# Performance work log

Hardware: AMD Instinct MI355X
Metric: run time of the kernel (lower is better)

The kernel has to match this reference:

```python
import jax, jax.numpy as jnp
import numpy as np

T, B, D_IN, H = 512, 128, 1024, 2048

def _lstm_cell(x, h, c, W_ih, W_hh, b):
    # PyTorch LSTMCell gate order: i, f, g, o
    gates = x @ W_ih.T + h @ W_hh.T + b  # [B, 4H]
    i, f, g, o = jnp.split(gates, 4, axis=-1)
    c_new = jax.nn.sigmoid(f) * c + jax.nn.sigmoid(i) * jnp.tanh(g)
    h_new = jax.nn.sigmoid(o) * jnp.tanh(c_new)
    return h_new, c_new

def setup_inputs() -> dict:
    key = jax.random.key(0)
    ks = jax.random.split(key, 12)
    k = 1.0 / np.sqrt(H)  # torch LSTMCell init range
    u = lambda kk, shape: jax.random.uniform(kk, shape, jnp.float32, -k, k)
    return {
        "input_seq": jax.random.normal(ks[0], (T, B, D_IN), jnp.float32),
        "h0": jax.random.normal(ks[1], (2, B, H), jnp.float32),
        "c0": jax.random.normal(ks[2], (2, B, H), jnp.float32),
        "W_ih0": u(ks[3], (4 * H, D_IN)),
        "W_hh0": u(ks[4], (4 * H, H)),
        "b0": u(ks[5], (4 * H,)),
        "W_ih1": u(ks[6], (4 * H, H)),
        "W_hh1": u(ks[7], (4 * H, H)),
        "b1": u(ks[8], (4 * H,)),
    }

def reference(input_seq, h0, c0, W_ih0, W_hh0, b0, W_ih1, W_hh1, b1):
    def step(carry, x_t):
        h0_, c0_, h1_, c1_ = carry
        h0n, c0n = _lstm_cell(x_t, h0_, c0_, W_ih0, W_hh0, b0)
        h1n, c1n = _lstm_cell(h0n, h1_, c1_, W_ih1, W_hh1, b1)
        return (h0n, c0n, h1n, c1n), None

    init = (h0[0], c0[0], h0[1], c0[1])
    (h0f, c0f, h1f, c1f), _ = jax.lax.scan(step, init, input_seq)
    return h1f  # last layer hidden at final timestep [B, H]
```

## Files before the change

kernel.cpp:

```cpp
#include <hip/hip_runtime.h>
#include <stdint.h>
#include <stddef.h>

#define T_STEPS 512
#define B_SZ    128
#define DIN     1024
#define H_SZ    2048
#define NG      8192
#define BH      (B_SZ * H_SZ)

typedef __attribute__((ext_vector_type(8))) short bf16x8;
typedef __attribute__((ext_vector_type(4))) float f32x4;

static __device__ __forceinline__ unsigned short f2bf(float x) {
  unsigned int u = __float_as_uint(x);
  u += 0x7fffu + ((u >> 16) & 1u);
  return (unsigned short)(u >> 16);
}

static __device__ __forceinline__ float sigm(float x) {
  return 1.0f / (1.0f + __expf(-x));
}
static __device__ __forceinline__ float tanh_(float x) {
  float e = __expf(-2.0f * fabsf(x));
  float t = (1.0f - e) / (1.0f + e);
  return x < 0.0f ? -t : t;
}

static __device__ __forceinline__ void async_load16(const void* gsrc, void* ldst) {
  __builtin_amdgcn_global_load_lds(
      (__attribute__((address_space(1))) void*)(const_cast<void*>(gsrc)),
      (__attribute__((address_space(3))) void*)ldst,
      16, 0, 0);
}

static __device__ __forceinline__ void wg_barrier_pinned() {
  __builtin_amdgcn_s_barrier();
  asm volatile("" ::: "memory");
  __builtin_amdgcn_sched_barrier(0);
}

__global__ void cvt_x_bf16(const float4* __restrict__ in, ushort4* __restrict__ out, int n4) {
  int i = blockIdx.x * blockDim.x + threadIdx.x;
  int st = gridDim.x * blockDim.x;
  for (; i < n4; i += st) {
    float4 v = in[i];
    ushort4 o;
    o.x = f2bf(v.x); o.y = f2bf(v.y); o.z = f2bf(v.z); o.w = f2bf(v.w);
    out[i] = o;
  }
}

__global__ void build_wcat(const float* __restrict__ wa, const float* __restrict__ wb,
                           unsigned short* __restrict__ outw, int ka, int K) {
  int k = blockIdx.x * blockDim.x + threadIdx.x;
  int n = blockIdx.y;
  if (k >= K) return;
  int kb = K - ka;
  float v = (k < ka) ? wa[(size_t)n * ka + k]
                     : wb[(size_t)n * kb + (k - ka)];
  outw[(size_t)n * K + k] = f2bf(v);
}

__global__ void init_state(const float* __restrict__ h0, const float* __restrict__ c0,
                           unsigned short* __restrict__ hb0, unsigned short* __restrict__ hb1,
                           float* __restrict__ cws) {
  int i = blockIdx.x * blockDim.x + threadIdx.x;
  if (i < BH) {
    hb0[i] = f2bf(h0[i]);
    hb1[i] = f2bf(h0[BH + i]);
    cws[i] = c0[i];
    cws[BH + i] = c0[BH + i];
  }
}

template<int K, int KSPLIT>
static __device__ __forceinline__ void lstm_step_body(
    unsigned short (*Bbuf)[64 * 64],
    const unsigned short* __restrict__ a0,
    const unsigned short* __restrict__ a1,
    const unsigned short* __restrict__ w,
    const float* __restrict__ bias,
    float* __restrict__ c,
    unsigned short* __restrict__ hout,
    float* __restrict__ fout,
    int tid, int lane, int wv, int n0)
{
  constexpr int KT = K >> 6;
  f32x4 acc[2][4] = {};

  const unsigned short* r0p[2];
  const unsigned short* r1p[2];
#pragma unroll
  for (int rt = 0; rt < 2; ++rt) {
    int row = wv * 32 + rt * 16 + (lane & 15);
    r0p[rt] = a0 + (size_t)row * KSPLIT;
    r1p[rt] = a1 + (size_t)row * H_SZ;
  }
  const int klo = (lane >> 4) << 3;

  auto loadA = [&](int kt, bf16x8 (&A)[2][2]) {
    const int kb = kt << 6;
    const bool sA = kb < KSPLIT;
    const int off = (sA ? kb : kb - KSPLIT) + klo;
#pragma unroll
    for (int rt = 0; rt < 2; ++rt) {
      const unsigned short* bp = (sA ? r0p[rt] : r1p[rt]) + off;
      A[rt][0] = *(const bf16x8*)(bp);
      A[rt][1] = *(const bf16x8*)(bp + 32);
    }
  };

  auto stageB = [&](int kt) {
    const int kb = kt << 6;
#pragma unroll
    for (int it = 0; it < 2; ++it) {
      int cid = it * 256 + tid;
      int nl  = cid >> 3;
      int chs = (cid & 7) ^ (nl & 7);
      int nn  = ((nl >> 4) << 11) + n0 + (nl & 15);
      const unsigned short* src = w + (size_t)nn * K + kb + (chs << 3);
      async_load16(src, &Bbuf[kt & 7][(it * 256 + wv * 64) * 8]);
    }
  };

  auto iter = [&](int kt, bf16x8 (&A)[2][2]) {
    if (kt + 7 < KT) stageB(kt + 7);
    const int bq = kt & 7;
#pragma unroll
    for (int kkk = 0; kkk < 2; ++kkk) {
      const int ch = kkk * 4 + (lane >> 4);
      const int cswz = (ch ^ (lane & 7)) << 3;
      bf16x8 bfr[4];
#pragma unroll
      for (int ct = 0; ct < 4; ++ct)
        bfr[ct] = *(const bf16x8*)&Bbuf[bq][(ct * 16 + (lane & 15)) * 64 + cswz];
#pragma unroll
      for (int rt = 0; rt < 2; ++rt)
#pragma unroll
        for (int ct = 0; ct < 4; ++ct)
          acc[rt][ct] = __builtin_amdgcn_mfma_f32_16x16x32_bf16(A[rt][kkk], bfr[ct], acc[rt][ct], 0, 0, 0);
    }
    if (kt + 4 < KT) loadA(kt + 4, A);
    int rem = KT - 1 - kt;
    if (rem >= 7)      asm volatile("s_waitcnt vmcnt(40)" ::: "memory");
    else if (rem == 6) asm volatile("s_waitcnt vmcnt(38)" ::: "memory");
    else if (rem == 5) asm volatile("s_waitcnt vmcnt(36)" ::: "memory");
    else if (rem == 4) asm volatile("s_waitcnt vmcnt(34)" ::: "memory");
    else if (rem == 3) asm volatile("s_waitcnt vmcnt(28)" ::: "memory");
    else if (rem == 2) asm volatile("s_waitcnt vmcnt(22)" ::: "memory");
    else if (rem == 1) asm volatile("s_waitcnt vmcnt(16)" ::: "memory");
    wg_barrier_pinned();
  };

  asm volatile("s_waitcnt vmcnt(0)" ::: "memory");

  bf16x8 A0[2][2], A1[2][2], A2[2][2], A3[2][2];
  stageB(0); loadA(0, A0);
  stageB(1); loadA(1, A1);
  stageB(2); loadA(2, A2);
  stageB(3); loadA(3, A3);
  stageB(4); stageB(5); stageB(6);
  asm volatile("s_waitcnt vmcnt(28)" ::: "memory");
  wg_barrier_pinned();

  for (int kt = 0; kt < KT; kt += 4) {
    iter(kt,     A0);
    iter(kt + 1, A1);
    iter(kt + 2, A2);
    iter(kt + 3, A3);
  }

  const int hc = n0 + (lane & 15);
  const float bi  = bias[hc];
  const float bff = bias[H_SZ + hc];
  const float bg  = bias[2 * H_SZ + hc];
  const float bo  = bias[3 * H_SZ + hc];

#pragma unroll
  for (int rt = 0; rt < 2; ++rt) {
#pragma unroll
    for (int r = 0; r < 4; ++r) {
      int row = wv * 32 + rt * 16 + ((lane >> 4) << 2) + r;
      size_t idx = (size_t)row * H_SZ + hc;
      float iv = sigm(acc[rt][0][r] + bi);
      float fv = sigm(acc[rt][1][r] + bff);
      float gv = tanh_(acc[rt][2][r] + bg);
      float ov = sigm(acc[rt][3][r] + bo);
      float cn = fv * c[idx] + iv * gv;
      c[idx] = cn;
      float hn = ov * tanh_(cn);
      hout[idx] = f2bf(hn);
      if (fout) fout[idx] = hn;
    }
  }
}

template<int K, int KSPLIT>
__global__ __launch_bounds__(256) void lstm_one(
    const unsigned short* __restrict__ a0, const unsigned short* __restrict__ a1,
    const unsigned short* __restrict__ w,  const float* __restrict__ bias,
    float* __restrict__ c, unsigned short* __restrict__ hout, float* __restrict__ fout)
{
  __shared__ __align__(16) unsigned short Bbuf[8][64 * 64];
  const int tid = threadIdx.x, lane = tid & 63, wv = tid >> 6, n0 = blockIdx.x << 4;
  lstm_step_body<K, KSPLIT>(Bbuf, a0, a1, w, bias, c, hout, fout, tid, lane, wv, n0);
}

template<int K1, int KS1, int K2, int KS2>
__global__ __launch_bounds__(256) void lstm_pair(
    const unsigned short* __restrict__ a0_1, const unsigned short* __restrict__ a1_1,
    const unsigned short* __restrict__ w1,   const float* __restrict__ bias1,
    float* __restrict__ c1, unsigned short* __restrict__ h1out,
    const unsigned short* __restrict__ a0_2, const unsigned short* __restrict__ a1_2,
    const unsigned short* __restrict__ w2,   const float* __restrict__ bias2,
    float* __restrict__ c2, unsigned short* __restrict__ h2out)
{
  __shared__ __align__(16) unsigned short Bbuf[8][64 * 64];
  const int tid = threadIdx.x, lane = tid & 63, wv = tid >> 6;
  if (blockIdx.x < 128) {
    const int n0 = blockIdx.x << 4;
    lstm_step_body<K1, KS1>(Bbuf, a0_1, a1_1, w1, bias1, c1, h1out, nullptr, tid, lane, wv, n0);
  } else {
    const int n0 = (blockIdx.x - 128) << 4;
    lstm_step_body<K2, KS2>(Bbuf, a0_2, a1_2, w2, bias2, c2, h2out, nullptr, tid, lane, wv, n0);
  }
}

extern "C" void kernel_launch(void* const* d_in, const int* in_sizes, int n_in,
                              void* d_out, int out_size, void* d_ws, size_t ws_size,
                              hipStream_t stream) {
  (void)in_sizes; (void)n_in; (void)out_size; (void)ws_size;
  const float* x    = (const float*)d_in[0];
  const float* h0   = (const float*)d_in[1];
  const float* c0   = (const float*)d_in[2];
  const float* Wih0 = (const float*)d_in[3];
  const float* Whh0 = (const float*)d_in[4];
  const float* b0   = (const float*)d_in[5];
  const float* Wih1 = (const float*)d_in[6];
  const float* Whh1 = (const float*)d_in[7];
  const float* b1   = (const float*)d_in[8];
  float* out = (float*)d_out;

  unsigned short* xbf = (unsigned short*)d_ws;
  unsigned short* Wc0 = xbf + (size_t)T_STEPS * B_SZ * DIN;
  unsigned short* Wc1 = Wc0 + (size_t)NG * 3072;
  unsigned short* hb0 = Wc1 + (size_t)NG * 4096;
  unsigned short* hb1 = hb0 + 2 * (size_t)BH;
  float*          cws = (float*)(hb1 + 2 * (size_t)BH);

  cvt_x_bf16<<<dim3(4096), dim3(256), 0, stream>>>(
      (const float4*)x, (ushort4*)xbf, T_STEPS * B_SZ * DIN / 4);
  build_wcat<<<dim3(12, NG), dim3(256), 0, stream>>>(Wih0, Whh0, Wc0, DIN, 3072);
  build_wcat<<<dim3(16, NG), dim3(256), 0, stream>>>(Wih1, Whh1, Wc1, H_SZ, 4096);
  init_state<<<dim3(BH / 256), dim3(256), 0, stream>>>(h0, c0, hb0, hb1, cws);

  lstm_one<3072, 1024><<<dim3(128), dim3(256), 0, stream>>>(
      xbf, hb0 + 0, Wc0, b0, cws, hb0 + BH, nullptr);

  for (int t = 0; t < T_STEPS - 1; ++t) {
    const unsigned short* h0cur = hb0 + (size_t)((t + 1) & 1) * BH;
    lstm_pair<4096, 2048, 3072, 1024><<<dim3(256), dim3(256), 0, stream>>>(
           h0cur, hb1 + (size_t)(t & 1) * BH, Wc1, b1,
                    cws + BH, hb1 + (size_t)((t + 1) & 1) * BH,
         xbf + (size_t)(t + 1) * B_SZ * DIN, h0cur, Wc0, b0,
                    cws, hb0 + (size_t)(t & 1) * BH);
  }
  lstm_one<4096, 2048><<<dim3(128), dim3(256), 0, stream>>>(
      hb0 + 0, hb1 + BH, Wc1, b1, cws + BH, hb1 + 0, out);
}
```

Baseline: 22.30 ms.

## Retile LSTM step blocks to 64 rows by 128 gate columns

```diff
diff --git a/kernel.cpp b/kernel.cpp
--- a/kernel.cpp
+++ b/kernel.cpp
@@ -76,7 +76,7 @@
 
 template<int K, int KSPLIT>
 static __device__ __forceinline__ void lstm_step_body(
-    unsigned short (*Bbuf)[64 * 64],
+    unsigned short (*Bbuf)[128 * 64],
     const unsigned short* __restrict__ a0,
     const unsigned short* __restrict__ a1,
     const unsigned short* __restrict__ w,
@@ -84,84 +84,69 @@
     float* __restrict__ c,
     unsigned short* __restrict__ hout,
     float* __restrict__ fout,
-    int tid, int lane, int wv, int n0)
+    int tid, int lane, int wv, int mb, int n0h)
 {
   constexpr int KT = K >> 6;
-  f32x4 acc[2][4] = {};
-
-  const unsigned short* r0p[2];
-  const unsigned short* r1p[2];
-#pragma unroll
-  for (int rt = 0; rt < 2; ++rt) {
-    int row = wv * 32 + rt * 16 + (lane & 15);
-    r0p[rt] = a0 + (size_t)row * KSPLIT;
-    r1p[rt] = a1 + (size_t)row * H_SZ;
-  }
+  f32x4 acc[8] = {};
+
+  const int arow = mb * 64 + wv * 16 + (lane & 15);
+  const unsigned short* r0p = a0 + (size_t)arow * KSPLIT;
+  const unsigned short* r1p = a1 + (size_t)arow * H_SZ;
   const int klo = (lane >> 4) << 3;
 
-  auto loadA = [&](int kt, bf16x8 (&A)[2][2]) {
+  auto loadA = [&](int kt, bf16x8 (&A)[2]) {
     const int kb = kt << 6;
     const bool sA = kb < KSPLIT;
-    const int off = (sA ? kb : kb - KSPLIT) + klo;
-#pragma unroll
-    for (int rt = 0; rt < 2; ++rt) {
-      const unsigned short* bp = (sA ? r0p[rt] : r1p[rt]) + off;
-      A[rt][0] = *(const bf16x8*)(bp);
-      A[rt][1] = *(const bf16x8*)(bp + 32);
-    }
+    const unsigned short* bp = (sA ? r0p : r1p) + (sA ? kb : kb - KSPLIT) + klo;
+    A[0] = *(const bf16x8*)(bp);
+    A[1] = *(const bf16x8*)(bp + 32);
   };
 
   auto stageB = [&](int kt) {
     const int kb = kt << 6;
 #pragma unroll
-    for (int it = 0; it < 2; ++it) {
+    for (int it = 0; it < 4; ++it) {
       int cid = it * 256 + tid;
       int nl  = cid >> 3;
       int chs = (cid & 7) ^ (nl & 7);
-      int nn  = ((nl >> 4) << 11) + n0 + (nl & 15);
+      int nn  = ((nl >> 5) << 11) + n0h + (nl & 31);
       const unsigned short* src = w + (size_t)nn * K + kb + (chs << 3);
-      async_load16(src, &Bbuf[kt & 7][(it * 256 + wv * 64) * 8]);
+      async_load16(src, &Bbuf[kt & 3][(it * 256 + wv * 64) * 8]);
     }
   };
 
-  auto iter = [&](int kt, bf16x8 (&A)[2][2]) {
-    if (kt + 7 < KT) stageB(kt + 7);
-    const int bq = kt & 7;
+  auto iter = [&](int kt, bf16x8 (&A)[2]) {
+    if (kt + 3 < KT) stageB(kt + 3);
+    const int bq = kt & 3;
 #pragma unroll
     for (int kkk = 0; kkk < 2; ++kkk) {
       const int ch = kkk * 4 + (lane >> 4);
       const int cswz = (ch ^ (lane & 7)) << 3;
-      bf16x8 bfr[4];
-#pragma unroll
-      for (int ct = 0; ct < 4; ++ct)
+      bf16x8 bfr[8];
+#pragma unroll
+      for (int ct = 0; ct < 8; ++ct)
         bfr[ct] = *(const bf16x8*)&Bbuf[bq][(ct * 16 + (lane & 15)) * 64 + cswz];
 #pragma unroll
-      for (int rt = 0; rt < 2; ++rt)
-#pragma unroll
-        for (int ct = 0; ct < 4; ++ct)
-          acc[rt][ct] = __builtin_amdgcn_mfma_f32_16x16x32_bf16(A[rt][kkk], bfr[ct], acc[rt][ct], 0, 0, 0);
+      for (int ct = 0; ct < 8; ++ct)
+        acc[ct] = __builtin_amdgcn_mfma_f32_16x16x32_bf16(A[kkk], bfr[ct], acc[ct], 0, 0, 0);
     }
     if (kt + 4 < KT) loadA(kt + 4, A);
     int rem = KT - 1 - kt;
-    if (rem >= 7)      asm volatile("s_waitcnt vmcnt(40)" ::: "memory");
-    else if (rem == 6) asm volatile("s_waitcnt vmcnt(38)" ::: "memory");
-    else if (rem == 5) asm volatile("s_waitcnt vmcnt(36)" ::: "memory");
-    else if (rem == 4) asm volatile("s_waitcnt vmcnt(34)" ::: "memory");
-    else if (rem == 3) asm volatile("s_waitcnt vmcnt(28)" ::: "memory");
-    else if (rem == 2) asm volatile("s_waitcnt vmcnt(22)" ::: "memory");
-    else if (rem == 1) asm volatile("s_waitcnt vmcnt(16)" ::: "memory");
+    if (rem >= 4)      asm volatile("s_waitcnt vmcnt(14)" ::: "memory");
+    else if (rem == 3) asm volatile("s_waitcnt vmcnt(12)" ::: "memory");
+    else if (rem == 2) asm volatile("s_waitcnt vmcnt(6)"  ::: "memory");
+    else if (rem == 1) asm volatile("s_waitcnt vmcnt(0)"  ::: "memory");
     wg_barrier_pinned();
   };
 
   asm volatile("s_waitcnt vmcnt(0)" ::: "memory");
 
-  bf16x8 A0[2][2], A1[2][2], A2[2][2], A3[2][2];
+  bf16x8 A0[2], A1[2], A2[2], A3[2];
   stageB(0); loadA(0, A0);
   stageB(1); loadA(1, A1);
   stageB(2); loadA(2, A2);
-  stageB(3); loadA(3, A3);
-  stageB(4); stageB(5); stageB(6);
-  asm volatile("s_waitcnt vmcnt(28)" ::: "memory");
+  loadA(3, A3);
+  asm volatile("s_waitcnt vmcnt(16)" ::: "memory");
   wg_barrier_pinned();
 
   for (int kt = 0; kt < KT; kt += 4) {
@@ -171,22 +156,21 @@
     iter(kt + 3, A3);
   }
 
-  const int hc = n0 + (lane & 15);
-  const float bi  = bias[hc];
-  const float bff = bias[H_SZ + hc];
-  const float bg  = bias[2 * H_SZ + hc];
-  const float bo  = bias[3 * H_SZ + hc];
-
-#pragma unroll
-  for (int rt = 0; rt < 2; ++rt) {
+#pragma unroll
+  for (int p = 0; p < 2; ++p) {
+    const int hc = n0h + p * 16 + (lane & 15);
+    const float bi  = bias[hc];
+    const float bff = bias[H_SZ + hc];
+    const float bg  = bias[2 * H_SZ + hc];
+    const float bo  = bias[3 * H_SZ + hc];
 #pragma unroll
     for (int r = 0; r < 4; ++r) {
-      int row = wv * 32 + rt * 16 + ((lane >> 4) << 2) + r;
+      int row = mb * 64 + wv * 16 + ((lane >> 4) << 2) + r;
       size_t idx = (size_t)row * H_SZ + hc;
-      float iv = sigm(acc[rt][0][r] + bi);
-      float fv = sigm(acc[rt][1][r] + bff);
-      float gv = tanh_(acc[rt][2][r] + bg);
-      float ov = sigm(acc[rt][3][r] + bo);
+      float iv = sigm(acc[p    ][r] + bi);
+      float fv = sigm(acc[p + 2][r] + bff);
+      float gv = tanh_(acc[p + 4][r] + bg);
+      float ov = sigm(acc[p + 6][r] + bo);
       float cn = fv * c[idx] + iv * gv;
       c[idx] = cn;
       float hn = ov * tanh_(cn);
@@ -202,9 +186,10 @@
     const unsigned short* __restrict__ w,  const float* __restrict__ bias,
     float* __restrict__ c, unsigned short* __restrict__ hout, float* __restrict__ fout)
 {
-  __shared__ __align__(16) unsigned short Bbuf[8][64 * 64];
-  const int tid = threadIdx.x, lane = tid & 63, wv = tid >> 6, n0 = blockIdx.x << 4;
-  lstm_step_body<K, KSPLIT>(Bbuf, a0, a1, w, bias, c, hout, fout, tid, lane, wv, n0);
+  __shared__ __align__(16) unsigned short Bbuf[4][128 * 64];
+  const int tid = threadIdx.x, lane = tid & 63, wv = tid >> 6;
+  const int mb = blockIdx.x >> 6, n0h = (blockIdx.x & 63) << 5;
+  lstm_step_body<K, KSPLIT>(Bbuf, a0, a1, w, bias, c, hout, fout, tid, lane, wv, mb, n0h);
 }
 
 template<int K1, int KS1, int K2, int KS2>
@@ -216,14 +201,15 @@
     const unsigned short* __restrict__ w2,   const float* __restrict__ bias2,
     float* __restrict__ c2, unsigned short* __restrict__ h2out)
 {
-  __shared__ __align__(16) unsigned short Bbuf[8][64 * 64];
+  __shared__ __align__(16) unsigned short Bbuf[4][128 * 64];
   const int tid = threadIdx.x, lane = tid & 63, wv = tid >> 6;
   if (blockIdx.x < 128) {
-    const int n0 = blockIdx.x << 4;
-    lstm_step_body<K1, KS1>(Bbuf, a0_1, a1_1, w1, bias1, c1, h1out, nullptr, tid, lane, wv, n0);
+    const int mb = blockIdx.x >> 6, n0h = (blockIdx.x & 63) << 5;
+    lstm_step_body<K1, KS1>(Bbuf, a0_1, a1_1, w1, bias1, c1, h1out, nullptr, tid, lane, wv, mb, n0h);
   } else {
-    const int n0 = (blockIdx.x - 128) << 4;
-    lstm_step_body<K2, KS2>(Bbuf, a0_2, a1_2, w2, bias2, c2, h2out, nullptr, tid, lane, wv, n0);
+    const int W = blockIdx.x - 128;
+    const int mb = W >> 6, n0h = (W & 63) << 5;
+    lstm_step_body<K2, KS2>(Bbuf, a0_2, a1_2, w2, bias2, c2, h2out, nullptr, tid, lane, wv, mb, n0h);
   }
 }
 
```

Result: faster. 19.93 ms (-10.6%).
